# Kernel optimization log

Measured on AMD Instinct MI355X. Metric: run time of the kernel, lower is better.

The kernel has to match this reference:

```python
import jax, jax.numpy as jnp
import numpy as np
import math

B, S, D, H = 2, 2048, 1024, 16
DK = D // H


def setup_inputs() -> dict:
    key = jax.random.key(0)
    ks = jax.random.split(key, 12)
    scale = 1.0 / math.sqrt(D)
    inp = {
        "q": jax.random.normal(ks[0], (B, S, D), jnp.float32),
        "k": jax.random.normal(ks[1], (B, S, D), jnp.float32),
        "v": jax.random.normal(ks[2], (B, S, D), jnp.float32),
        # causal mask, broadcast over batch and heads; 0 entries are masked out
        "mask": jnp.tril(jnp.ones((S, S), jnp.int32))[None, None, :, :],
        "wq_w": jax.random.normal(ks[3], (D, D), jnp.float32) * scale,
        "wq_b": jax.random.normal(ks[4], (D,), jnp.float32) * 0.01,
        "wk_w": jax.random.normal(ks[5], (D, D), jnp.float32) * scale,
        "wk_b": jax.random.normal(ks[6], (D,), jnp.float32) * 0.01,
        "wv_w": jax.random.normal(ks[7], (D, D), jnp.float32) * scale,
        "wv_b": jax.random.normal(ks[8], (D,), jnp.float32) * 0.01,
        "wo_w": jax.random.normal(ks[9], (D, D), jnp.float32) * scale,
        "wo_b": jax.random.normal(ks[10], (D,), jnp.float32) * 0.01,
    }
    return inp


def _mha(q, k, v, mask, wq_w, wq_b, wk_w, wk_b, wv_w, wv_b, wo_w, wo_b):
    # nn.Linear: x @ W^T + b
    def split_heads(x):  # [B,S,D] -> [B,H,S,DK]
        return x.reshape(B, S, H, DK).transpose(0, 2, 1, 3)

    Q = split_heads(q @ wq_w.T + wq_b)
    K = split_heads(k @ wk_w.T + wk_b)
    V = split_heads(v @ wv_w.T + wv_b)

    scores = jnp.einsum("bhqd,bhkd->bhqk", Q, K) / math.sqrt(DK)  # [B,H,S,S]
    scores = jnp.where(mask == 0, jnp.float32(-1e9), scores)
    # NOTE: source uses softmax(dim=1) == over the HEADS axis; replicated faithfully.
    attn = jax.nn.softmax(scores, axis=1)
    out = jnp.einsum("bhqk,bhkd->bhqd", attn, V)  # [B,H,S,DK]
    out = out.transpose(0, 2, 1, 3).reshape(B, S, D)
    return out @ wo_w.T + wo_b


def reference(q, k, v, mask, wq_w, wq_b, wk_w, wk_b, wv_w, wv_b, wo_w, wo_b):
    return _mha(q, k, v, mask, wq_w, wq_b, wk_w, wk_b, wv_w, wv_b, wo_w, wo_b)
```

## Files before the change

### kernel.cpp

```cpp
#include <hip/hip_runtime.h>
#include <stdint.h>


#define BB 2
#define SS 2048
#define DD 1024
#define HH 16
#define DKK 64

typedef _Float16 f16;
typedef __attribute__((ext_vector_type(2))) _Float16 f16x2;
typedef __attribute__((ext_vector_type(8))) _Float16 f16x8;
typedef __attribute__((ext_vector_type(2))) __fp16 fp16x2_raw;
typedef __attribute__((ext_vector_type(4))) float f32x4;

typedef __attribute__((address_space(3))) uint32_t lds32_t;
typedef __attribute__((address_space(1))) uint32_t g32_t;

__device__ __forceinline__ void async_cp16(void* lds, const void* g){
    __builtin_amdgcn_global_load_lds((const g32_t*)g, (lds32_t*)lds, 16, 0, 0);
}

union U32H { uint32_t u; f16x2 h; fp16x2_raw hr; };

__device__ __forceinline__ uint32_t pk2(float a, float b){
    U32H c; c.hr = __builtin_amdgcn_cvt_pkrtz(a, b); return c.u;
}
__device__ __forceinline__ float h_lo(uint32_t w){ U32H c; c.u = w; return (float)c.h[0]; }
__device__ __forceinline__ float h_hi(uint32_t w){ U32H c; c.u = w; return (float)c.h[1]; }
__device__ __forceinline__ uint32_t pkmul(uint32_t a, uint32_t b){
    U32H x, y, r; x.u = a; y.u = b; r.h = x.h * y.h; return r.u;
}
__device__ __forceinline__ uint16_t f2h(float f){
    union { f16 h; uint16_t u; } c; c.h = (f16)f; return c.u;
}

__global__ __launch_bounds__(256) void cvt_all(
    const float* __restrict__ w0, const float* __restrict__ w1,
    const float* __restrict__ w2, const float* __restrict__ w3,
    const float* __restrict__ a0, const float* __restrict__ a1,
    const float* __restrict__ a2,
    uint16_t* __restrict__ dw0, uint16_t* __restrict__ dw1,
    uint16_t* __restrict__ dw2, uint16_t* __restrict__ dw3,
    uint16_t* __restrict__ da0, uint16_t* __restrict__ da1,
    uint16_t* __restrict__ da2)
{
    const int y = blockIdx.y;
    const float* s; uint16_t* d; int n4;
    switch (y) {
        case 0: s = w0; d = dw0; n4 = 262144; break;
        case 1: s = w1; d = dw1; n4 = 262144; break;
        case 2: s = w2; d = dw2; n4 = 262144; break;
        case 3: s = w3; d = dw3; n4 = 262144; break;
        case 4: s = a0; d = da0; n4 = 1048576; break;
        case 5: s = a1; d = da1; n4 = 1048576; break;
        default: s = a2; d = da2; n4 = 1048576; break;
    }
    int i = blockIdx.x * 256 + threadIdx.x;
    if (i >= n4) return;
    float4 v = ((const float4*)s)[i];
    ((uint2*)d)[i] = make_uint2(pk2(v.x, v.y), pk2(v.z, v.w));
}

template <int OMODE>
__device__ __forceinline__ void gemm_core(
    uint16_t (*As)[32], uint16_t (*Bs)[32],
    const uint16_t* __restrict__ A, const uint16_t* __restrict__ W,
    const float* __restrict__ bias, void* __restrict__ Cout,
    const int kbeg, const int kend)
{
    const int t    = threadIdx.x;
    const int bm   = blockIdx.x * 128;
    const int bn   = blockIdx.y * 128;
    const int lane = t & 63;
    const int w    = t >> 6;
    const int wm   = (w >> 1) * 64;
    const int wn   = (w & 1) * 64;
    const int lm   = lane & 15;
    const int quad = lane >> 4;

    f32x4 acc[4][4] = {};

    const int lr = lane >> 2;
    const int lc = (lane & 3) * 8;

    for (int k0 = kbeg; k0 < kend; k0 += 32) {
#pragma unroll
        for (int i2 = 0; i2 < 2; ++i2) {
            const int i = w * 2 + i2;
            async_cp16(&As[16*i][0], &A[(size_t)(bm + 16*i + lr) * DD + k0 + lc]);
            async_cp16(&Bs[16*i][0], &W[(size_t)(bn + 16*i + lr) * DD + k0 + lc]);
        }
        __syncthreads();
        f16x8 a8[4], b8[4];
#pragma unroll
        for (int mt = 0; mt < 4; ++mt) a8[mt] = *(const f16x8*)&As[wm + 16*mt + lm][quad*8];
#pragma unroll
        for (int nt = 0; nt < 4; ++nt) b8[nt] = *(const f16x8*)&Bs[wn + 16*nt + lm][quad*8];
#pragma unroll
        for (int mt = 0; mt < 4; ++mt)
#pragma unroll
            for (int nt = 0; nt < 4; ++nt)
                acc[mt][nt] = __builtin_amdgcn_mfma_f32_16x16x32_f16(a8[mt], b8[nt], acc[mt][nt], 0, 0, 0);
        __syncthreads();
    }

#pragma unroll
    for (int nt = 0; nt < 4; ++nt) {
        const int ng = bn + wn + 16*nt + lm;
        const float bv = bias ? bias[ng] : 0.0f;
#pragma unroll
        for (int mt = 0; mt < 4; ++mt) {
            const int m0 = bm + wm + 16*mt + quad*4;
            if (OMODE == 1) {
                const int bb = m0 >> 11, s0 = m0 & (SS - 1);
                const int hh = ng >> 6,  dk = ng & 63;
                uint2 wv;
                wv.x = pk2(acc[mt][nt][0] + bv, acc[mt][nt][1] + bv);
                wv.y = pk2(acc[mt][nt][2] + bv, acc[mt][nt][3] + bv);
                *(uint2*)&((uint16_t*)Cout)[(((size_t)(bb*HH + hh))*DKK + dk)*SS + s0] = wv;
            } else {
#pragma unroll
                for (int r = 0; r < 4; ++r) {
                    const int m = m0 + r;
                    const float val = acc[mt][nt][r] + bv;
                    if (OMODE == 0) {
                        const int bb = m >> 11, s = m & (SS - 1);
                        const int hh = ng >> 6, dk = ng & 63;
                        ((uint16_t*)Cout)[(((size_t)(bb*HH + hh))*SS + s)*DKK + dk] = f2h(val);
                    } else {
                        ((float*)Cout)[(size_t)m * DD + ng] = val;
                    }
                }
            }
        }
    }
}

__global__ __launch_bounds__(256) void gemm_qkv(
    const uint16_t* __restrict__ xq, const uint16_t* __restrict__ wq,
    const float* __restrict__ bq, uint16_t* __restrict__ Qc,
    const uint16_t* __restrict__ xk, const uint16_t* __restrict__ wk,
    const float* __restrict__ bk, uint16_t* __restrict__ Kc,
    const uint16_t* __restrict__ xv, const uint16_t* __restrict__ wv,
    const float* __restrict__ bv, uint16_t* __restrict__ Vt)
{
    __shared__ __align__(16) uint16_t As[128][32];
    __shared__ __align__(16) uint16_t Bs[128][32];
    const int z = blockIdx.z;
    if (z == 0)      gemm_core<0>(As, Bs, xq, wq, bq, Qc, 0, DD);
    else if (z == 1) gemm_core<0>(As, Bs, xk, wk, bk, Kc, 0, DD);
    else             gemm_core<1>(As, Bs, xv, wv, bv, Vt, 0, DD);
}

__global__ __launch_bounds__(256) void gemm_o_split(
    const uint16_t* __restrict__ A, const uint16_t* __restrict__ W,
    const float* __restrict__ bias, float* __restrict__ P0, float* __restrict__ P1)
{
    __shared__ __align__(16) uint16_t As[128][32];
    __shared__ __align__(16) uint16_t Bs[128][32];
    const int z = blockIdx.z;
    if (z == 0) gemm_core<2>(As, Bs, A, W, bias,    (void*)P0, 0,   512);
    else        gemm_core<2>(As, Bs, A, W, nullptr, (void*)P1, 512, 1024);
}

__global__ __launch_bounds__(256) void addf4(
    const float* __restrict__ a, const float* __restrict__ b, float* __restrict__ o)
{
    const int i = blockIdx.x * 256 + threadIdx.x;
    float4 x = ((const float4*)a)[i];
    float4 y = ((const float4*)b)[i];
    ((float4*)o)[i] = make_float4(x.x+y.x, x.y+y.y, x.z+y.z, x.w+y.w);
}

__global__ __launch_bounds__(256) void suf_kernel(
    const uint16_t* __restrict__ Vt, float* __restrict__ Suf)
{
    const int bh = blockIdx.x;
    const int t  = threadIdx.x;
    const int d = t & 63, seg = t >> 6;
    __shared__ float cs[64][65];
    const uint16_t* row = Vt + ((size_t)bh * DKK + d) * SS;
    for (int cl = 0; cl < 16; ++cl) {
        const int c = seg * 16 + cl;
        float sum = 0.f;
#pragma unroll
        for (int jj = 0; jj < 4; ++jj) {
            uint4 u = *(const uint4*)&row[c * 32 + jj * 8];
            sum += ((h_lo(u.x)+h_hi(u.x)) + (h_lo(u.y)+h_hi(u.y)))
                 + ((h_lo(u.z)+h_hi(u.z)) + (h_lo(u.w)+h_hi(u.w)));
        }
        cs[c][d] = sum;
    }
    __syncthreads();
    if (t < 64) {
        float run = 0.f;
        Suf[((size_t)bh * 65 + 64) * DKK + t] = 0.f;
        for (int c = 63; c >= 0; --c) {
            run += cs[c][t];
            Suf[((size_t)bh * 65 + c) * DKK + t] = run;
        }
    }
}

__global__ __launch_bounds__(1024) void attn_v9(
    const uint16_t* __restrict__ Qc, const uint16_t* __restrict__ Kc,
    const uint16_t* __restrict__ Vt, const float* __restrict__ Suf,
    uint16_t* __restrict__ AOp)
{
    __shared__ __align__(16) uint16_t E[3][16][32][40];
    __shared__ __align__(16) uint16_t Zr[2][32][40];

    const int x  = blockIdx.x;
    const int p  = x & 3;
    const int b  = (x >> 2) & 1;
    const int pr = x >> 3;
    const int tid  = threadIdx.x;
    const int h    = tid >> 6;
    const int lane = tid & 63;
    const int lm   = lane & 15;
    const int quad = lane >> 4;

    const uint16_t* Qh = Qc + ((size_t)(b*HH + h)) * SS * DKK;
    const uint16_t* Kh = Kc + ((size_t)(b*HH + h)) * SS * DKK;
    const uint16_t* Vh = Vt + ((size_t)(b*HH + h)) * DKK * SS;
    uint16_t* AOb = AOp + ((size_t)(p*BB + b)) * SS * DD;

    const int rq  = tid >> 4;
    const int rk2 = tid & 15;

#pragma unroll
    for (int tt = 0; tt < 2; ++tt) {
        const int tq = tt ? (63 - pr) : pr;
        const int q0 = tq * 32;
        const int nch = (tq >= p) ? ((tq - p) >> 2) + 1 : 0;

        f16x8 qf[2][2];
#pragma unroll
        for (int qt = 0; qt < 2; ++qt)
#pragma unroll
            for (int kd = 0; kd < 2; ++kd)
                qf[qt][kd] = *(const f16x8*)&Qh[(size_t)(q0 + 16*qt + lm)*DKK + kd*32 + quad*8];

        f32x4 oacc[2][4] = {};

        auto SCORES = [&](int c, int ebw) {
            const int k0 = c * 32;
            f32x4 sacc[2][2] = {};
#pragma unroll
            for (int kt = 0; kt < 2; ++kt) {
                f16x8 kf0 = *(const f16x8*)&Kh[(size_t)(k0 + 16*kt + lm)*DKK + quad*8];
                f16x8 kf1 = *(const f16x8*)&Kh[(size_t)(k0 + 16*kt + lm)*DKK + 32 + quad*8];
#pragma unroll
                for (int qt = 0; qt < 2; ++qt) {
                    sacc[kt][qt] = __builtin_amdgcn_mfma_f32_16x16x32_f16(kf0, qf[qt][0], sacc[kt][qt], 0, 0, 0);
                    sacc[kt][qt] = __builtin_amdgcn_mfma_f32_16x16x32_f16(kf1, qf[qt][1], sacc[kt][qt], 0, 0, 0);
                }
            }
#pragma unroll
            for (int kt = 0; kt < 2; ++kt)
#pragma unroll
                for (int qt = 0; qt < 2; ++qt) {
                    const int qg = q0 + 16*qt + lm;
                    float e[4];
#pragma unroll
                    for (int r = 0; r < 4; ++r) {
                        const int kg = k0 + 16*kt + quad*4 + r;
                        e[r] = (kg > qg) ? 1.0f : __expf(sacc[kt][qt][r] * 0.125f);
                    }
                    *(uint2*)&E[ebw][h][16*qt + lm][16*kt + quad*4] =
                        make_uint2(pk2(e[0], e[1]), pk2(e[2], e[3]));
                }
        };

        auto HEADSUM = [&](int ebr, int zbw) {
            float z0 = 0.f, z1 = 0.f;
#pragma unroll
            for (int i = 0; i < 16; ++i) {
                uint32_t wv2 = *(const uint32_t*)&E[ebr][i][rq][rk2*2];
                z0 += h_lo(wv2); z1 += h_hi(wv2);
            }
            *(uint32_t*)&Zr[zbw][rq][rk2*2] = pk2(__fdividef(1.f, z0), __fdividef(1.f, z1));
        };

        auto PV = [&](int c, int ebr, int zbr) {
            const int k0 = c * 32;
            f16x8 vf[4];
#pragma unroll
            for (int dt = 0; dt < 4; ++dt)
                vf[dt] = *(const f16x8*)&Vh[(size_t)(16*dt + lm)*SS + k0 + quad*8];
#pragma unroll
            for (int qt = 0; qt < 2; ++qt) {
                uint4 eu = *(const uint4*)&E[ebr][h][16*qt + lm][quad*8];
                uint4 zu = *(const uint4*)&Zr[zbr][16*qt + lm][quad*8];
                union { uint4 u; f16x8 v; } P;
                P.u.x = pkmul(eu.x, zu.x); P.u.y = pkmul(eu.y, zu.y);
                P.u.z = pkmul(eu.z, zu.z); P.u.w = pkmul(eu.w, zu.w);
#pragma unroll
                for (int dt = 0; dt < 4; ++dt)
                    oacc[qt][dt] = __builtin_amdgcn_mfma_f32_16x16x32_f16(P.v, vf[dt], oacc[qt][dt], 0, 0, 0);
            }
        };

        __syncthreads();

        if (nch > 0) {
            SCORES(p, 0);
            __syncthreads();
            int eb = 0;
            for (int n = 0; n < nch; ++n) {
                const int c  = p + 4*n;
                const int zb = n & 1;
                if (tid < 512) HEADSUM(eb, zb);
                if (n > 0)       PV(c - 4, (eb + 2) % 3, zb ^ 1);
                if (n + 1 < nch) SCORES(c + 4, (eb + 1) % 3);
                __syncthreads();
                eb = (eb + 1 == 3) ? 0 : eb + 1;
            }
            PV(p + 4*(nch - 1), (eb + 2) % 3, (nch - 1) & 1);
        }

        float corr[4] = {0.f, 0.f, 0.f, 0.f};
        if (p == 0) {
            const float* Sf = Suf + ((size_t)(b*HH + h) * 65 + (tq + 1)) * DKK;
#pragma unroll
            for (int dt = 0; dt < 4; ++dt) corr[dt] = 0.0625f * Sf[16*dt + lm];
        }
#pragma unroll
        for (int qt = 0; qt < 2; ++qt)
#pragma unroll
            for (int dt = 0; dt < 4; ++dt)
#pragma unroll
                for (int r = 0; r < 4; ++r) {
                    const int s = q0 + 16*qt + quad*4 + r;
                    AOb[(size_t)s * DD + h*DKK + 16*dt + lm] = f2h(oacc[qt][dt][r] + corr[dt]);
                }
    }
}

__global__ __launch_bounds__(256) void reduce4(uint16_t* AOp)
{
    const size_t P1 = (size_t)BB * SS * DD;
    const int i = blockIdx.x * 256 + threadIdx.x;
    uint2 u0 = ((const uint2*)AOp)[i];
    uint2 u1 = ((const uint2*)(AOp + P1))[i];
    uint2 u2 = ((const uint2*)(AOp + 2*P1))[i];
    uint2 u3 = ((const uint2*)(AOp + 3*P1))[i];
    float r0 = (h_lo(u0.x) + h_lo(u1.x)) + (h_lo(u2.x) + h_lo(u3.x));
    float r1 = (h_hi(u0.x) + h_hi(u1.x)) + (h_hi(u2.x) + h_hi(u3.x));
    float r2 = (h_lo(u0.y) + h_lo(u1.y)) + (h_lo(u2.y) + h_lo(u3.y));
    float r3 = (h_hi(u0.y) + h_hi(u1.y)) + (h_hi(u2.y) + h_hi(u3.y));
    ((uint2*)AOp)[i] = make_uint2(pk2(r0, r1), pk2(r2, r3));
}

extern "C" void kernel_launch(void* const* d_in, const int* in_sizes, int n_in,
                              void* d_out, int out_size, void* d_ws, size_t ws_size,
                              hipStream_t stream)
{
    const float* q    = (const float*)d_in[0];
    const float* k    = (const float*)d_in[1];
    const float* v    = (const float*)d_in[2];
    const float* wq_w = (const float*)d_in[4];
    const float* wq_b = (const float*)d_in[5];
    const float* wk_w = (const float*)d_in[6];
    const float* wk_b = (const float*)d_in[7];
    const float* wv_w = (const float*)d_in[8];
    const float* wv_b = (const float*)d_in[9];
    const float* wo_w = (const float*)d_in[10];
    const float* wo_b = (const float*)d_in[11];
    float* out = (float*)d_out;

    uint16_t* wsu = (uint16_t*)d_ws;
    const size_t M1 = (size_t)1 << 20;
    uint16_t* wcq = wsu + 0 * M1;
    uint16_t* wck = wsu + 1 * M1;
    uint16_t* wcv = wsu + 2 * M1;
    uint16_t* wco = wsu + 3 * M1;
    uint16_t* Qc  = wsu + 4 * M1;
    uint16_t* Kc  = wsu + 8 * M1;
    uint16_t* Vt  = wsu + 12 * M1;
    uint16_t* AOp = wsu + 16 * M1;
    uint16_t* xq  = wsu + 16 * M1;
    uint16_t* xk  = wsu + 20 * M1;
    uint16_t* xv  = wsu + 24 * M1;
    float*    Suf = (float*)wcq;
    float*    P0  = (float*)(wsu + 20 * M1);
    float*    P1  = (float*)(wsu + 8 * M1);

    cvt_all<<<dim3(4096, 7), 256, 0, stream>>>(
        wq_w, wk_w, wv_w, wo_w, q, k, v,
        wcq, wck, wcv, wco, xq, xk, xv);

    gemm_qkv<<<dim3(32, 8, 3), 256, 0, stream>>>(
        xq, wcq, wq_b, Qc,
        xk, wck, wk_b, Kc,
        xv, wcv, wv_b, Vt);

    suf_kernel<<<32, 256, 0, stream>>>(Vt, Suf);
    attn_v9<<<256, 1024, 0, stream>>>(Qc, Kc, Vt, Suf, AOp);

    reduce4<<<4096, 256, 0, stream>>>(AOp);
    gemm_o_split<<<dim3(32, 8, 2), 256, 0, stream>>>(AOp, wco, wo_b, P0, P1);
    addf4<<<4096, 256, 0, stream>>>(P0, P1, out);
}
```

Baseline: 286.2 us.

## Hoist K/V global loads ahead of compute and specialize causal mask tiles

Moves the K and V fragment loads to the top of each pipeline iteration, so global memory latency overlaps the head-sum and MFMA work. Adds a fast path in score exponentiation for tiles that are fully below or above the diagonal, skipping per-element mask checks. The head-sum reduction now uses packed fp16 adds in a tree instead of fp32 accumulation. This cuts ALU work but accumulates the softmax denominator in half precision, which may lose accuracy, and holding loads in flight raises register pressure.

Measured after the change: 298.1 us. +4.2%, slower.

```diff
diff --git a/kernel.cpp b/kernel.cpp
--- a/kernel.cpp
+++ b/kernel.cpp
@@ -30,6 +30,9 @@
 __device__ __forceinline__ float h_hi(uint32_t w){ U32H c; c.u = w; return (float)c.h[1]; }
 __device__ __forceinline__ uint32_t pkmul(uint32_t a, uint32_t b){
     U32H x, y, r; x.u = a; y.u = b; r.h = x.h * y.h; return r.u;
+}
+__device__ __forceinline__ uint32_t pkadd(uint32_t a, uint32_t b){
+    U32H x, y, r; x.u = a; y.u = b; r.h = x.h + y.h; return r.u;
 }
 __device__ __forceinline__ uint16_t f2h(float f){
     union { f16 h; uint16_t u; } c; c.h = (f16)f; return c.u;
@@ -203,7 +206,7 @@
     }
 }
 
-__global__ __launch_bounds__(1024) void attn_v9(
+__global__ __launch_bounds__(1024) void attn_v10(
     const uint16_t* __restrict__ Qc, const uint16_t* __restrict__ Kc,
     const uint16_t* __restrict__ Vt, const float* __restrict__ Suf,
     uint16_t* __restrict__ AOp)
@@ -244,51 +247,70 @@
 
         f32x4 oacc[2][4] = {};
 
-        auto SCORES = [&](int c, int ebw) {
+        auto LOADK = [&](int c, f16x8* kf) {
+            const int k0 = c * 32;
+#pragma unroll
+            for (int kt = 0; kt < 2; ++kt) {
+                kf[2*kt+0] = *(const f16x8*)&Kh[(size_t)(k0 + 16*kt + lm)*DKK + quad*8];
+                kf[2*kt+1] = *(const f16x8*)&Kh[(size_t)(k0 + 16*kt + lm)*DKK + 32 + quad*8];
+            }
+        };
+        auto LOADV = [&](int c, f16x8* vf) {
+            const int k0 = c * 32;
+#pragma unroll
+            for (int dt = 0; dt < 4; ++dt)
+                vf[dt] = *(const f16x8*)&Vh[(size_t)(16*dt + lm)*SS + k0 + quad*8];
+        };
+
+        auto SCORES_C = [&](int c, int ebw, const f16x8* kf) {
             const int k0 = c * 32;
             f32x4 sacc[2][2] = {};
 #pragma unroll
-            for (int kt = 0; kt < 2; ++kt) {
-                f16x8 kf0 = *(const f16x8*)&Kh[(size_t)(k0 + 16*kt + lm)*DKK + quad*8];
-                f16x8 kf1 = *(const f16x8*)&Kh[(size_t)(k0 + 16*kt + lm)*DKK + 32 + quad*8];
+            for (int kt = 0; kt < 2; ++kt)
 #pragma unroll
                 for (int qt = 0; qt < 2; ++qt) {
-                    sacc[kt][qt] = __builtin_amdgcn_mfma_f32_16x16x32_f16(kf0, qf[qt][0], sacc[kt][qt], 0, 0, 0);
-                    sacc[kt][qt] = __builtin_amdgcn_mfma_f32_16x16x32_f16(kf1, qf[qt][1], sacc[kt][qt], 0, 0, 0);
+                    sacc[kt][qt] = __builtin_amdgcn_mfma_f32_16x16x32_f16(kf[2*kt+0], qf[qt][0], sacc[kt][qt], 0, 0, 0);
+                    sacc[kt][qt] = __builtin_amdgcn_mfma_f32_16x16x32_f16(kf[2*kt+1], qf[qt][1], sacc[kt][qt], 0, 0, 0);
                 }
-            }
 #pragma unroll
             for (int kt = 0; kt < 2; ++kt)
 #pragma unroll
                 for (int qt = 0; qt < 2; ++qt) {
-                    const int qg = q0 + 16*qt + lm;
-                    float e[4];
-#pragma unroll
-                    for (int r = 0; r < 4; ++r) {
-                        const int kg = k0 + 16*kt + quad*4 + r;
-                        e[r] = (kg > qg) ? 1.0f : __expf(sacc[kt][qt][r] * 0.125f);
+                    const int kh = k0 + 16*kt, qh = q0 + 16*qt;
+                    uint2 evw;
+                    if (kh + 15 <= qh) {
+                        evw.x = pk2(__expf(sacc[kt][qt][0] * 0.125f), __expf(sacc[kt][qt][1] * 0.125f));
+                        evw.y = pk2(__expf(sacc[kt][qt][2] * 0.125f), __expf(sacc[kt][qt][3] * 0.125f));
+                    } else if (kh > qh + 15) {
+                        evw.x = 0x3C003C00u; evw.y = 0x3C003C00u;
+                    } else {
+                        const int qg = qh + lm;
+                        float e[4];
+#pragma unroll
+                        for (int r = 0; r < 4; ++r) {
+                            const int kg = kh + quad*4 + r;
+                            e[r] = (kg > qg) ? 1.0f : __expf(sacc[kt][qt][r] * 0.125f);
+                        }
+                        evw = make_uint2(pk2(e[0], e[1]), pk2(e[2], e[3]));
                     }
-                    *(uint2*)&E[ebw][h][16*qt + lm][16*kt + quad*4] =
-                        make_uint2(pk2(e[0], e[1]), pk2(e[2], e[3]));
+                    *(uint2*)&E[ebw][h][16*qt + lm][16*kt + quad*4] = evw;
                 }
         };
 
         auto HEADSUM = [&](int ebr, int zbw) {
-            float z0 = 0.f, z1 = 0.f;
-#pragma unroll
-            for (int i = 0; i < 16; ++i) {
-                uint32_t wv2 = *(const uint32_t*)&E[ebr][i][rq][rk2*2];
-                z0 += h_lo(wv2); z1 += h_hi(wv2);
-            }
-            *(uint32_t*)&Zr[zbw][rq][rk2*2] = pk2(__fdividef(1.f, z0), __fdividef(1.f, z1));
+            uint32_t t8[8];
+#pragma unroll
+            for (int i = 0; i < 8; ++i)
+                t8[i] = pkadd(*(const uint32_t*)&E[ebr][i][rq][rk2*2],
+                              *(const uint32_t*)&E[ebr][i+8][rq][rk2*2]);
+            uint32_t s0 = pkadd(pkadd(t8[0], t8[4]), pkadd(t8[1], t8[5]));
+            uint32_t s1 = pkadd(pkadd(t8[2], t8[6]), pkadd(t8[3], t8[7]));
+            uint32_t s  = pkadd(s0, s1);
+            *(uint32_t*)&Zr[zbw][rq][rk2*2] =
+                pk2(__fdividef(1.f, h_lo(s)), __fdividef(1.f, h_hi(s)));
         };
 
-        auto PV = [&](int c, int ebr, int zbr) {
-            const int k0 = c * 32;
-            f16x8 vf[4];
-#pragma unroll
-            for (int dt = 0; dt < 4; ++dt)
-                vf[dt] = *(const f16x8*)&Vh[(size_t)(16*dt + lm)*SS + k0 + quad*8];
+        auto PV = [&](int ebr, int zbr, const f16x8* vf) {
 #pragma unroll
             for (int qt = 0; qt < 2; ++qt) {
                 uint4 eu = *(const uint4*)&E[ebr][h][16*qt + lm][quad*8];
@@ -305,19 +327,30 @@
         __syncthreads();
 
         if (nch > 0) {
-            SCORES(p, 0);
+            {
+                f16x8 kf[4];
+                LOADK(p, kf);
+                SCORES_C(p, 0, kf);
+            }
             __syncthreads();
             int eb = 0;
             for (int n = 0; n < nch; ++n) {
                 const int c  = p + 4*n;
                 const int zb = n & 1;
-                if (tid < 512) HEADSUM(eb, zb);
-                if (n > 0)       PV(c - 4, (eb + 2) % 3, zb ^ 1);
-                if (n + 1 < nch) SCORES(c + 4, (eb + 1) % 3);
+                f16x8 vf[4], kf[4];
+                if (n > 0)       LOADV(c - 4, vf);
+                if (n + 1 < nch) LOADK(c + 4, kf);
+                if (tid < 512)   HEADSUM(eb, zb);
+                if (n + 1 < nch) SCORES_C(c + 4, (eb + 1) % 3, kf);
+                if (n > 0)       PV((eb + 2) % 3, zb ^ 1, vf);
                 __syncthreads();
                 eb = (eb + 1 == 3) ? 0 : eb + 1;
             }
-            PV(p + 4*(nch - 1), (eb + 2) % 3, (nch - 1) & 1);
+            {
+                f16x8 vf[4];
+                LOADV(p + 4*(nch - 1), vf);
+                PV((eb + 2) % 3, (nch - 1) & 1, vf);
+            }
         }
 
         float corr[4] = {0.f, 0.f, 0.f, 0.f};
@@ -397,7 +430,7 @@
         xv, wcv, wv_b, Vt);
 
     suf_kernel<<<32, 256, 0, stream>>>(Vt, Suf);
-    attn_v9<<<256, 1024, 0, stream>>>(Qc, Kc, Vt, Suf, AOp);
+    attn_v10<<<256, 1024, 0, stream>>>(Qc, Kc, Vt, Suf, AOp);
 
     reduce4<<<4096, 256, 0, stream>>>(AOp);
     gemm_o_split<<<dim3(32, 8, 2), 256, 0, stream>>>(AOp, wco, wo_b, P0, P1);
```

## Fuse partial-sum reduction into output GEMM load and trim launch overheads

Applied to the files above, without the earlier changes.

Drops the separate reduce4 kernel. The output-projection GEMM now reads the four fp16 attention partials and sums them with packed fp16 adds before staging the A tile in LDS, instead of using async LDS copies. cvt_all moves to a flat grid with no idle blocks, suf_kernel uses 1024 threads, and partial P0 is written straight into the output buffer to skip an intermediate. Risks are a loss of precision from summing in fp16 rather than fp32, and synchronous loads in the GEMM loop that read each partial twice across the two split-K halves.

Result: no change. 291.2 us (+1.7%).

```diff
diff --git a/kernel.cpp b/kernel.cpp
--- a/kernel.cpp
+++ b/kernel.cpp
@@ -30,6 +30,9 @@
 __device__ __forceinline__ float h_hi(uint32_t w){ U32H c; c.u = w; return (float)c.h[1]; }
 __device__ __forceinline__ uint32_t pkmul(uint32_t a, uint32_t b){
     U32H x, y, r; x.u = a; y.u = b; r.h = x.h * y.h; return r.u;
+}
+__device__ __forceinline__ uint32_t pkadd(uint32_t a, uint32_t b){
+    U32H x, y, r; x.u = a; y.u = b; r.h = x.h + y.h; return r.u;
 }
 __device__ __forceinline__ uint16_t f2h(float f){
     union { f16 h; uint16_t u; } c; c.h = (f16)f; return c.u;
@@ -45,24 +48,25 @@
     uint16_t* __restrict__ da0, uint16_t* __restrict__ da1,
     uint16_t* __restrict__ da2)
 {
-    const int y = blockIdx.y;
-    const float* s; uint16_t* d; int n4;
-    switch (y) {
-        case 0: s = w0; d = dw0; n4 = 262144; break;
-        case 1: s = w1; d = dw1; n4 = 262144; break;
-        case 2: s = w2; d = dw2; n4 = 262144; break;
-        case 3: s = w3; d = dw3; n4 = 262144; break;
-        case 4: s = a0; d = da0; n4 = 1048576; break;
-        case 5: s = a1; d = da1; n4 = 1048576; break;
-        default: s = a2; d = da2; n4 = 1048576; break;
-    }
-    int i = blockIdx.x * 256 + threadIdx.x;
-    if (i >= n4) return;
+    const int id = blockIdx.x;
+    const float* s; uint16_t* d; int i;
+    if (id < 4096) {
+        const int y = id >> 10;
+        s = (y==0) ? w0 : (y==1) ? w1 : (y==2) ? w2 : w3;
+        d = (y==0) ? dw0 : (y==1) ? dw1 : (y==2) ? dw2 : dw3;
+        i = (id & 1023) * 256 + threadIdx.x;
+    } else {
+        const int id2 = id - 4096;
+        const int y = id2 >> 12;
+        s = (y==0) ? a0 : (y==1) ? a1 : a2;
+        d = (y==0) ? da0 : (y==1) ? da1 : da2;
+        i = (id2 & 4095) * 256 + threadIdx.x;
+    }
     float4 v = ((const float4*)s)[i];
     ((uint2*)d)[i] = make_uint2(pk2(v.x, v.y), pk2(v.z, v.w));
 }
 
-template <int OMODE>
+template <int OMODE, int SUMA>
 __device__ __forceinline__ void gemm_core(
     uint16_t (*As)[32], uint16_t (*Bs)[32],
     const uint16_t* __restrict__ A, const uint16_t* __restrict__ W,
@@ -83,12 +87,27 @@
 
     const int lr = lane >> 2;
     const int lc = (lane & 3) * 8;
+    const size_t PS = (size_t)BB * SS * DD;
 
     for (int k0 = kbeg; k0 < kend; k0 += 32) {
 #pragma unroll
         for (int i2 = 0; i2 < 2; ++i2) {
             const int i = w * 2 + i2;
-            async_cp16(&As[16*i][0], &A[(size_t)(bm + 16*i + lr) * DD + k0 + lc]);
+            const size_t aoff = (size_t)(bm + 16*i + lr) * DD + k0 + lc;
+            if (SUMA) {
+                uint4 u0 = *(const uint4*)&A[aoff];
+                uint4 u1 = *(const uint4*)&A[aoff + PS];
+                uint4 u2 = *(const uint4*)&A[aoff + 2*PS];
+                uint4 u3 = *(const uint4*)&A[aoff + 3*PS];
+                uint4 sm;
+                sm.x = pkadd(pkadd(u0.x, u1.x), pkadd(u2.x, u3.x));
+                sm.y = pkadd(pkadd(u0.y, u1.y), pkadd(u2.y, u3.y));
+                sm.z = pkadd(pkadd(u0.z, u1.z), pkadd(u2.z, u3.z));
+                sm.w = pkadd(pkadd(u0.w, u1.w), pkadd(u2.w, u3.w));
+                *(uint4*)&As[16*i + lr][lc] = sm;
+            } else {
+                async_cp16(&As[16*i][0], &A[aoff]);
+            }
             async_cp16(&Bs[16*i][0], &W[(size_t)(bn + 16*i + lr) * DD + k0 + lc]);
         }
         __syncthreads();
@@ -148,9 +167,9 @@
     __shared__ __align__(16) uint16_t As[128][32];
     __shared__ __align__(16) uint16_t Bs[128][32];
     const int z = blockIdx.z;
-    if (z == 0)      gemm_core<0>(As, Bs, xq, wq, bq, Qc, 0, DD);
-    else if (z == 1) gemm_core<0>(As, Bs, xk, wk, bk, Kc, 0, DD);
-    else             gemm_core<1>(As, Bs, xv, wv, bv, Vt, 0, DD);
+    if (z == 0)      gemm_core<0,0>(As, Bs, xq, wq, bq, Qc, 0, DD);
+    else if (z == 1) gemm_core<0,0>(As, Bs, xk, wk, bk, Kc, 0, DD);
+    else             gemm_core<1,0>(As, Bs, xv, wv, bv, Vt, 0, DD);
 }
 
 __global__ __launch_bounds__(256) void gemm_o_split(
@@ -160,8 +179,8 @@
     __shared__ __align__(16) uint16_t As[128][32];
     __shared__ __align__(16) uint16_t Bs[128][32];
     const int z = blockIdx.z;
-    if (z == 0) gemm_core<2>(As, Bs, A, W, bias,    (void*)P0, 0,   512);
-    else        gemm_core<2>(As, Bs, A, W, nullptr, (void*)P1, 512, 1024);
+    if (z == 0) gemm_core<2,1>(As, Bs, A, W, bias,    (void*)P0, 0,   512);
+    else        gemm_core<2,1>(As, Bs, A, W, nullptr, (void*)P1, 512, 1024);
 }
 
 __global__ __launch_bounds__(256) void addf4(
@@ -173,7 +192,7 @@
     ((float4*)o)[i] = make_float4(x.x+y.x, x.y+y.y, x.z+y.z, x.w+y.w);
 }
 
-__global__ __launch_bounds__(256) void suf_kernel(
+__global__ __launch_bounds__(1024) void suf_kernel(
     const uint16_t* __restrict__ Vt, float* __restrict__ Suf)
 {
     const int bh = blockIdx.x;
@@ -181,8 +200,9 @@
     const int d = t & 63, seg = t >> 6;
     __shared__ float cs[64][65];
     const uint16_t* row = Vt + ((size_t)bh * DKK + d) * SS;
-    for (int cl = 0; cl < 16; ++cl) {
-        const int c = seg * 16 + cl;
+#pragma unroll
+    for (int cl = 0; cl < 4; ++cl) {
+        const int c = seg * 4 + cl;
         float sum = 0.f;
 #pragma unroll
         for (int jj = 0; jj < 4; ++jj) {
@@ -336,21 +356,6 @@
                     AOb[(size_t)s * DD + h*DKK + 16*dt + lm] = f2h(oacc[qt][dt][r] + corr[dt]);
                 }
     }
-}
-
-__global__ __launch_bounds__(256) void reduce4(uint16_t* AOp)
-{
-    const size_t P1 = (size_t)BB * SS * DD;
-    const int i = blockIdx.x * 256 + threadIdx.x;
-    uint2 u0 = ((const uint2*)AOp)[i];
-    uint2 u1 = ((const uint2*)(AOp + P1))[i];
-    uint2 u2 = ((const uint2*)(AOp + 2*P1))[i];
-    uint2 u3 = ((const uint2*)(AOp + 3*P1))[i];
-    float r0 = (h_lo(u0.x) + h_lo(u1.x)) + (h_lo(u2.x) + h_lo(u3.x));
-    float r1 = (h_hi(u0.x) + h_hi(u1.x)) + (h_hi(u2.x) + h_hi(u3.x));
-    float r2 = (h_lo(u0.y) + h_lo(u1.y)) + (h_lo(u2.y) + h_lo(u3.y));
-    float r3 = (h_hi(u0.y) + h_hi(u1.y)) + (h_hi(u2.y) + h_hi(u3.y));
-    ((uint2*)AOp)[i] = make_uint2(pk2(r0, r1), pk2(r2, r3));
 }
 
 extern "C" void kernel_launch(void* const* d_in, const int* in_sizes, int n_in,
@@ -384,10 +389,9 @@
     uint16_t* xk  = wsu + 20 * M1;
     uint16_t* xv  = wsu + 24 * M1;
     float*    Suf = (float*)wcq;
-    float*    P0  = (float*)(wsu + 20 * M1);
-    float*    P1  = (float*)(wsu + 8 * M1);
-
-    cvt_all<<<dim3(4096, 7), 256, 0, stream>>>(
+    float*    P1  = (float*)(wsu + 4 * M1);
+
+    cvt_all<<<16384, 256, 0, stream>>>(
         wq_w, wk_w, wv_w, wo_w, q, k, v,
         wcq, wck, wcv, wco, xq, xk, xv);
 
@@ -396,10 +400,9 @@
         xk, wck, wk_b, Kc,
         xv, wcv, wv_b, Vt);
 
-    suf_kernel<<<32, 256, 0, stream>>>(Vt, Suf);
+    suf_kernel<<<32, 1024, 0, stream>>>(Vt, Suf);
     attn_v9<<<256, 1024, 0, stream>>>(Qc, Kc, Vt, Suf, AOp);
 
-    reduce4<<<4096, 256, 0, stream>>>(AOp);
-    gemm_o_split<<<dim3(32, 8, 2), 256, 0, stream>>>(AOp, wco, wo_b, P0, P1);
-    addf4<<<4096, 256, 0, stream>>>(P0, P1, out);
-}
+    gemm_o_split<<<dim3(32, 8, 2), 256, 0, stream>>>(AOp, wco, wo_b, out, P1);
+    addf4<<<4096, 256, 0, stream>>>(out, P1, out);
+}
```
